# Kernel optimization log

Hardware: AMD Instinct MI355X
Metric: run time of the kernel (lower is better)

Reference implementation:

```python
import jax, jax.numpy as jnp
import numpy as np
from jax import lax

EPS = 1e-5  # GroupNorm eps (torch default)

def _silu(x):
    return x * jax.nn.sigmoid(x)

def _conv1x1(x, w, b):
    # x: (N, Ci, H, W), w: (Co, Ci), b: (Co,)
    return jnp.einsum('oi,nihw->nohw', w, x) + b[None, :, None, None]

def _conv3x3(x, w, b):
    # x: (N, Ci, H, W), w: (Co, Ci, 3, 3)
    y = lax.conv_general_dilated(x, w, window_strides=(1, 1), padding='SAME',
                                 dimension_numbers=('NCHW', 'OIHW', 'NCHW'))
    return y + b[None, :, None, None]

def setup_inputs() -> dict:
    key = jax.random.key(0)
    ks = jax.random.split(key, 6)
    B, C, H, W = 32, 512, 64, 64
    cg = 16
    return {
        'x': jax.random.normal(ks[0], (B, C, H, W), dtype=jnp.float32),
        'w1': jax.random.normal(ks[1], (cg, cg), dtype=jnp.float32) * 0.1,
        'b1': jnp.zeros((cg,), jnp.float32),
        'wh': jax.random.normal(ks[2], (cg, cg), dtype=jnp.float32) * 0.1,
        'bh': jnp.zeros((cg,), jnp.float32),
        'ww': jax.random.normal(ks[3], (cg, cg), dtype=jnp.float32) * 0.1,
        'bw': jnp.zeros((cg,), jnp.float32),
        'w3': jax.random.normal(ks[4], (cg, cg, 3, 3), dtype=jnp.float32) * 0.1,
        'b3': jnp.zeros((cg,), jnp.float32),
        'gamma': jnp.ones((cg,), jnp.float32),
        'beta': jnp.zeros((cg,), jnp.float32),
    }

def reference(x, w1, b1, wh, bh, ww, bw, w3, b3, gamma, beta):
    b, c, h, w = x.shape
    cg = w1.shape[0]
    g = c // cg
    n = b * g
    hw = h * w
    xg = x.reshape(n, cg, h, w)
    # directional pooling: (N, cg, H, 1) and (N, cg, W, 1)
    x_h = jnp.mean(xg, axis=3, keepdims=True)
    x_w = jnp.transpose(jnp.mean(xg, axis=2, keepdims=True), (0, 1, 3, 2))
    y = jnp.concatenate([x_h, x_w], axis=2)            # (N, cg, H+W, 1)
    y = _silu(_conv1x1(y, w1, b1))
    y_h, y_w = y[:, :, :h, :], y[:, :, h:, :]
    y_w = jnp.transpose(y_w, (0, 1, 3, 2))             # (N, cg, 1, W)
    a_h = jax.nn.sigmoid(_conv1x1(y_h, wh, bh))        # (N, cg, H, 1)
    a_w = jax.nn.sigmoid(_conv1x1(y_w, ww, bw))        # (N, cg, 1, W)
    x1 = xg * a_h * a_w
    # GroupNorm(num_groups=1): normalize over (cg, H, W) per sample
    mu = jnp.mean(x1, axis=(1, 2, 3), keepdims=True)
    var = jnp.var(x1, axis=(1, 2, 3), keepdims=True)
    x1 = (x1 - mu) * lax.rsqrt(var + EPS)
    x1 = x1 * gamma[None, :, None, None] + beta[None, :, None, None]
    x3 = _silu(_conv3x3(xg, w3, b3))
    A1 = jax.nn.softmax(x1.reshape(n, cg, hw), axis=-1)
    A3 = jax.nn.softmax(x3.reshape(n, cg, hw), axis=-1)
    v1 = jnp.mean(x1, axis=(2, 3))                     # (N, cg)
    v3 = jnp.mean(x3, axis=(2, 3))                     # (N, cg)
    s1 = jnp.einsum('nc,ncp->np', v1, A3)              # (N, HW)
    s2 = jnp.einsum('nc,ncp->np', v3, A1)
    s = jax.nn.sigmoid(s1 + s2).reshape(n, 1, h, w)
    out = (xg * s).reshape(b, c, h, w)
    return out
```

## Files before the change

### kernel.cpp

```cpp
#include <hip/hip_runtime.h>


typedef short bf16x8 __attribute__((ext_vector_type(8)));
typedef float f32x4 __attribute__((ext_vector_type(4)));

__device__ __forceinline__ unsigned short f2bf(float f) {
    union { float f; unsigned int u; } v; v.f = f;
    unsigned int u = v.u;
    u += 0x7fffu + ((u >> 16) & 1u);
    return (unsigned short)(u >> 16);
}
__device__ __forceinline__ float bf2f(unsigned short h) {
    union { unsigned int u; float f; } v; v.u = ((unsigned int)h) << 16;
    return v.f;
}
__device__ __forceinline__ float sigm(float v) { return 1.0f / (1.0f + __expf(-v)); }

#define XIDX(h1,w1,c) ((((h1)*2 + ((c)>>3))*66 + (w1))*8 + ((c)&7))

__global__ __launch_bounds__(512) void ema_fused(
    const float* __restrict__ x,
    const float* __restrict__ w1, const float* __restrict__ b1,
    const float* __restrict__ wh, const float* __restrict__ bh,
    const float* __restrict__ ww, const float* __restrict__ bw,
    const float* __restrict__ w3, const float* __restrict__ b3,
    const float* __restrict__ gamma, const float* __restrict__ beta,
    float* __restrict__ out)
{
    const int n   = blockIdx.x;
    const int tid = threadIdx.x;
    const int lane = tid & 63;
    const int wv   = tid >> 6;
    const int qd   = lane >> 4;
    const int col  = lane & 15;

    const float* xg = x + (size_t)n * 65536;
    unsigned int* ob = (unsigned int*)out + (size_t)n * 65536;

    __shared__ unsigned short sX[69696];
    __shared__ float sG[2048];
    __shared__ float sRedA[128], sRedB[128], sRedC[128], sRedD[128];
    __shared__ float sS1[16], sSQ[16], sMn[16], sMx[16], sM3[16], sS3[16];
    __shared__ float sA[16], sB1[16], sQ1[16], sQ3[16];
    __shared__ float sScal[2];

    for (int i = tid; i < 34848; i += 512) ((unsigned int*)sX)[i] = 0u;
    __syncthreads();
    for (int e = tid; e < 32768; e += 512) {
        int c2 = e & 7, w = (e >> 3) & 63, r = e >> 9;
        float v0 = xg[(2*c2)*4096 + r*64 + w];
        float v1 = xg[(2*c2+1)*4096 + r*64 + w];
        unsigned int pk = (unsigned int)f2bf(v0) | ((unsigned int)f2bf(v1) << 16);
        ((unsigned int*)sX)[XIDX(r+1, w+1, 2*c2) >> 1] = pk;
    }
    __syncthreads();

    if (tid < 256) {
        int half = tid & 1;
        int idx  = tid >> 1;
        int isCol = idx >> 6;
        int rc = idx & 63;
        float acc[8] = {0,0,0,0,0,0,0,0};
        for (int t = 0; t < 64; ++t) {
            int hh = isCol ? (t + 1) : (rc + 1);
            int wwi = isCol ? (rc + 1) : (t + 1);
            const bf16x8 v = *(const bf16x8*)&sX[XIDX(hh, wwi, half*8)];
            #pragma unroll
            for (int j = 0; j < 8; ++j) acc[j] += bf2f((unsigned short)v[j]);
        }
        #pragma unroll
        for (int j = 0; j < 8; ++j)
            sG[isCol*1024 + (half*8+j)*64 + rc] = acc[j] * (1.0f/64.0f);
    }
    __syncthreads();

    {
        float yv[4];
        #pragma unroll
        for (int j = 0; j < 4; ++j) {
            int tsk = tid + j*512;
            int o = tsk & 15, q = tsk >> 4;
            float acc = b1[o];
            #pragma unroll
            for (int i = 0; i < 16; ++i)
                acc += w1[o*16 + i] * sG[((q>>6)<<10) + i*64 + (q & 63)];
            yv[j] = acc * sigm(acc);
        }
        __syncthreads();
        #pragma unroll
        for (int j = 0; j < 4; ++j) {
            int tsk = tid + j*512;
            int o = tsk & 15, q = tsk >> 4;
            sG[o*128 + q] = yv[j];
        }
    }
    __syncthreads();
    {
        float av[4];
        #pragma unroll
        for (int j = 0; j < 4; ++j) {
            int tsk = tid + j*512;
            int kind = tsk >> 10;
            int o = tsk & 15, pos = (tsk >> 4) & 63;
            const float* wm = kind ? ww : wh;
            float acc = kind ? bw[o] : bh[o];
            #pragma unroll
            for (int i = 0; i < 16; ++i)
                acc += wm[o*16 + i] * sG[i*128 + kind*64 + pos];
            av[j] = sigm(acc);
        }
        __syncthreads();
        #pragma unroll
        for (int j = 0; j < 4; ++j) {
            int tsk = tid + j*512;
            int kind = tsk >> 10, o = tsk & 15, pos = (tsk >> 4) & 63;
            sG[kind*1024 + o*64 + pos] = av[j];
        }
    }
    __syncthreads();

    {
        bf16x8 afr[5];
        int offs[5];
        #pragma unroll
        for (int mm = 0; mm < 5; ++mm) {
            int t = 2*mm + (qd >> 1);
            #pragma unroll
            for (int j = 0; j < 8; ++j) {
                int i = ((qd & 1) << 3) + j;
                float v = (t <= 8) ? w3[(col*16 + i)*9 + t] : 0.0f;
                afr[mm][j] = (short)f2bf(v);
            }
            int tb = (t > 8) ? 8 : t;
            int dy = tb/3 - 1, dx = tb - (tb/3)*3 - 1;
            offs[mm] = dy*1056 + dx*8;
        }
        float b3v[4];
        #pragma unroll
        for (int r = 0; r < 4; ++r) b3v[r] = b3[qd*4 + r];

        float tmax[4] = {-1e30f,-1e30f,-1e30f,-1e30f};
        float tsum[4] = {0.f,0.f,0.f,0.f};

        for (int k = 0; k < 32; ++k) {
            int tile = wv*32 + k;
            int h = tile >> 2, wq = tile & 3;
            int base = XIDX(h+1, wq*16 + col + 1, (qd & 1)*8);
            f32x4 acc = {0.f, 0.f, 0.f, 0.f};
            #pragma unroll
            for (int mm = 0; mm < 5; ++mm) {
                const bf16x8 bfr = *(const bf16x8*)&sX[base + offs[mm]];
                acc = __builtin_amdgcn_mfma_f32_16x16x32_bf16(afr[mm], bfr, acc, 0, 0, 0);
            }
            int p = h*64 + wq*16 + col;
            float xv[4];
            #pragma unroll
            for (int r = 0; r < 4; ++r) {
                float v = acc[r] + b3v[r];
                float sv = v * sigm(v);
                xv[r] = sv;
                tmax[r] = fmaxf(tmax[r], sv);
                tsum[r] += sv;
            }
            unsigned int u0 = (unsigned int)f2bf(xv[0]) | ((unsigned int)f2bf(xv[1]) << 16);
            unsigned int u1 = (unsigned int)f2bf(xv[2]) | ((unsigned int)f2bf(xv[3]) << 16);
            ob[(4*qd)*4096 + p]     = u0;
            ob[(4*qd + 2)*4096 + p] = u1;
        }
        #pragma unroll
        for (int m = 1; m < 16; m <<= 1) {
            #pragma unroll
            for (int r = 0; r < 4; ++r) {
                tmax[r] = fmaxf(tmax[r], __shfl_xor(tmax[r], m, 64));
                tsum[r] += __shfl_xor(tsum[r], m, 64);
            }
        }
        if (col == 0) {
            #pragma unroll
            for (int r = 0; r < 4; ++r) {
                sRedA[wv*16 + qd*4 + r] = tmax[r];
                sRedB[wv*16 + qd*4 + r] = tsum[r];
            }
        }
    }
    __syncthreads();
    if (tid < 16) {
        float mx = -1e30f, sm = 0.f;
        for (int v2 = 0; v2 < 8; ++v2) { mx = fmaxf(mx, sRedA[v2*16 + tid]); sm += sRedB[v2*16 + tid]; }
        sM3[tid] = mx; sS3[tid] = sm;
    }
    __syncthreads();

    {
        int half = tid & 1;
        int wq4  = (tid >> 1) & 3;
        int r    = tid >> 3;
        float ah8[8];
        #pragma unroll
        for (int j = 0; j < 8; ++j) ah8[j] = sG[(half*8+j)*64 + r];
        float s1[8], q1[8], mn[8], mx[8];
        #pragma unroll
        for (int j = 0; j < 8; ++j) { s1[j]=0.f; q1[j]=0.f; mn[j]=1e30f; mx[j]=-1e30f; }
        for (int wi = 0; wi < 16; ++wi) {
            int w = wq4*16 + wi;
            const bf16x8 v = *(const bf16x8*)&sX[XIDX(r+1, w+1, half*8)];
            #pragma unroll
            for (int j = 0; j < 8; ++j) {
                float aw = sG[1024 + (half*8+j)*64 + w];
                float x1 = bf2f((unsigned short)v[j]) * ah8[j] * aw;
                s1[j] += x1; q1[j] += x1*x1;
                mn[j] = fminf(mn[j], x1); mx[j] = fmaxf(mx[j], x1);
            }
        }
        #pragma unroll
        for (int m = 2; m < 64; m <<= 1) {
            #pragma unroll
            for (int j = 0; j < 8; ++j) {
                s1[j] += __shfl_xor(s1[j], m, 64);
                q1[j] += __shfl_xor(q1[j], m, 64);
                mn[j] = fminf(mn[j], __shfl_xor(mn[j], m, 64));
                mx[j] = fmaxf(mx[j], __shfl_xor(mx[j], m, 64));
            }
        }
        if ((lane >> 1) == 0) {
            #pragma unroll
            for (int j = 0; j < 8; ++j) {
                int c = half*8 + j;
                sRedA[wv*16 + c] = s1[j];
                sRedB[wv*16 + c] = q1[j];
                sRedC[wv*16 + c] = mn[j];
                sRedD[wv*16 + c] = mx[j];
            }
        }
    }
    __syncthreads();
    if (tid < 16) {
        float s=0.f, q=0.f, mn=1e30f, mx=-1e30f;
        for (int v2 = 0; v2 < 8; ++v2) {
            s += sRedA[v2*16+tid]; q += sRedB[v2*16+tid];
            mn = fminf(mn, sRedC[v2*16+tid]); mx = fmaxf(mx, sRedD[v2*16+tid]);
        }
        sS1[tid]=s; sSQ[tid]=q; sMn[tid]=mn; sMx[tid]=mx;
    }
    __syncthreads();
    if (tid == 0) {
        float S=0.f, Q=0.f;
        for (int c = 0; c < 16; ++c) { S += sS1[c]; Q += sSQ[c]; }
        float mu = S * (1.0f/65536.0f);
        float var = Q * (1.0f/65536.0f) - mu*mu;
        sScal[0] = mu; sScal[1] = rsqrtf(var + 1e-5f);
    }
    __syncthreads();
    if (tid < 16) {
        float mu = sScal[0], rstd = sScal[1];
        float a  = gamma[tid] * rstd;
        float bb = beta[tid] - mu * a;
        float m1 = (a >= 0.f) ? (a*sMx[tid] + bb) : (a*sMn[tid] + bb);
        sA[tid]  = a;
        sB1[tid] = bb - m1;
        sMn[tid] = a * (sS1[tid] * (1.0f/4096.0f)) + bb;
        sMx[tid] = sS3[tid] * (1.0f/4096.0f);
    }
    __syncthreads();

    {
        float z1[16], z3[16];
        #pragma unroll
        for (int c = 0; c < 16; ++c) { z1[c]=0.f; z3[c]=0.f; }
        for (int pp = 0; pp < 8; ++pp) {
            int p = pp*512 + tid;
            int h = p >> 6, w = p & 63;
            const bf16x8 v0 = *(const bf16x8*)&sX[XIDX(h+1, w+1, 0)];
            const bf16x8 v1 = *(const bf16x8*)&sX[XIDX(h+1, w+1, 8)];
            unsigned int xq[8];
            #pragma unroll
            for (int c2 = 0; c2 < 8; ++c2) xq[c2] = ob[(2*c2)*4096 + p];
            #pragma unroll
            for (int c = 0; c < 16; ++c) {
                float xv = bf2f((unsigned short)((c < 8) ? v0[c] : v1[c-8]));
                float g = sG[c*64 + h] * sG[1024 + c*64 + w];
                z1[c] += __expf(xv*g*sA[c] + sB1[c]);
                unsigned short ub = (unsigned short)((c & 1) ? (xq[c>>1] >> 16) : (xq[c>>1] & 0xffffu));
                z3[c] += __expf(bf2f(ub) - sM3[c]);
            }
        }
        #pragma unroll
        for (int m = 1; m < 64; m <<= 1) {
            #pragma unroll
            for (int c = 0; c < 16; ++c) {
                z1[c] += __shfl_xor(z1[c], m, 64);
                z3[c] += __shfl_xor(z3[c], m, 64);
            }
        }
        if (lane == 0) {
            #pragma unroll
            for (int c = 0; c < 16; ++c) { sRedA[wv*16 + c] = z1[c]; sRedB[wv*16 + c] = z3[c]; }
        }
    }
    __syncthreads();
    if (tid < 16) {
        float a1=0.f, a3=0.f;
        for (int v2 = 0; v2 < 8; ++v2) { a1 += sRedA[v2*16+tid]; a3 += sRedB[v2*16+tid]; }
        sQ1[tid] = sMx[tid] / a1;
        sQ3[tid] = sMn[tid] / a3;
    }
    __syncthreads();

    for (int pp = 0; pp < 8; ++pp) {
        int p = pp*512 + tid;
        int h = p >> 6, w = p & 63;
        const bf16x8 v0 = *(const bf16x8*)&sX[XIDX(h+1, w+1, 0)];
        const bf16x8 v1 = *(const bf16x8*)&sX[XIDX(h+1, w+1, 8)];
        unsigned int xq[8];
        #pragma unroll
        for (int c2 = 0; c2 < 8; ++c2) xq[c2] = ob[(2*c2)*4096 + p];
        float xf[16];
        #pragma unroll
        for (int c = 0; c < 16; ++c) xf[c] = xg[c*4096 + p];
        float z = 0.f;
        #pragma unroll
        for (int c = 0; c < 16; ++c) {
            float xv = bf2f((unsigned short)((c < 8) ? v0[c] : v1[c-8]));
            float g = sG[c*64 + h] * sG[1024 + c*64 + w];
            float e1 = __expf(xv*g*sA[c] + sB1[c]);
            unsigned short ub = (unsigned short)((c & 1) ? (xq[c>>1] >> 16) : (xq[c>>1] & 0xffffu));
            float e3 = __expf(bf2f(ub) - sM3[c]);
            z += sQ3[c]*e3 + sQ1[c]*e1;
        }
        float s = 1.0f / (1.0f + __expf(-z));
        #pragma unroll
        for (int c = 0; c < 16; ++c)
            ob[c*4096 + p] = __float_as_uint(xf[c] * s);
    }
}

extern "C" void kernel_launch(void* const* d_in, const int* in_sizes, int n_in,
                              void* d_out, int out_size, void* d_ws, size_t ws_size,
                              hipStream_t stream) {
    const float* x     = (const float*)d_in[0];
    const float* w1    = (const float*)d_in[1];
    const float* b1    = (const float*)d_in[2];
    const float* wh    = (const float*)d_in[3];
    const float* bh    = (const float*)d_in[4];
    const float* ww    = (const float*)d_in[5];
    const float* bw    = (const float*)d_in[6];
    const float* w3    = (const float*)d_in[7];
    const float* b3    = (const float*)d_in[8];
    const float* gamma = (const float*)d_in[9];
    const float* beta  = (const float*)d_in[10];
    hipLaunchKernelGGL(ema_fused, dim3(1024), dim3(512), 0, stream,
                       x, w1, b1, wh, bh, ww, bw, w3, b3, gamma, beta, (float*)d_out);
}
```

Baseline: 725.3 us.

## Recompute 3x3 conv via MFMA instead of spilling bf16 x3 to global; 1024-thread blocks

The conv3x3+SiLU result is no longer written to the output buffer as bf16 and re-read twice. Instead the MFMA convolution is recomputed from LDS in the softmax-denominator pass and the final pass. Block size doubles to 1024 threads, with the pooling and reductions split across more threads. A transposed padded sAW table avoids bank conflicts. This trades extra MFMA work for removing global round-trips, at the cost of register pressure under the larger block.

Result: slower. 751.4 us (+3.6%).

```diff
diff --git a/kernel.cpp b/kernel.cpp
--- a/kernel.cpp
+++ b/kernel.cpp
@@ -2,6 +2,7 @@
 
 
 typedef short bf16x8 __attribute__((ext_vector_type(8)));
+typedef short bf16x4 __attribute__((ext_vector_type(4)));
 typedef float f32x4 __attribute__((ext_vector_type(4)));
 
 __device__ __forceinline__ unsigned short f2bf(float f) {
@@ -18,7 +19,7 @@
 
 #define XIDX(h1,w1,c) ((((h1)*2 + ((c)>>3))*66 + (w1))*8 + ((c)&7))
 
-__global__ __launch_bounds__(512) void ema_fused(
+__global__ __launch_bounds__(1024, 4) void ema_fused(
     const float* __restrict__ x,
     const float* __restrict__ w1, const float* __restrict__ b1,
     const float* __restrict__ wh, const float* __restrict__ bh,
@@ -33,20 +34,24 @@
     const int wv   = tid >> 6;
     const int qd   = lane >> 4;
     const int col  = lane & 15;
+    const int cBase = qd * 4;
 
     const float* xg = x + (size_t)n * 65536;
     unsigned int* ob = (unsigned int*)out + (size_t)n * 65536;
 
     __shared__ unsigned short sX[69696];
     __shared__ float sG[2048];
-    __shared__ float sRedA[128], sRedB[128], sRedC[128], sRedD[128];
+    __shared__ float sAW[1088];
+    __shared__ float sRedA[256], sRedB[256], sRedC[256], sRedD[256];
     __shared__ float sS1[16], sSQ[16], sMn[16], sMx[16], sM3[16], sS3[16];
     __shared__ float sA[16], sB1[16], sQ1[16], sQ3[16];
     __shared__ float sScal[2];
 
-    for (int i = tid; i < 34848; i += 512) ((unsigned int*)sX)[i] = 0u;
-    __syncthreads();
-    for (int e = tid; e < 32768; e += 512) {
+    for (int i = tid; i < 34848; i += 1024) ((unsigned int*)sX)[i] = 0u;
+    __syncthreads();
+    #pragma unroll
+    for (int it = 0; it < 32; ++it) {
+        int e = tid + it * 1024;
         int c2 = e & 7, w = (e >> 3) & 63, r = e >> 9;
         float v0 = xg[(2*c2)*4096 + r*64 + w];
         float v1 = xg[(2*c2+1)*4096 + r*64 + w];
@@ -55,30 +60,37 @@
     }
     __syncthreads();
 
-    if (tid < 256) {
-        int half = tid & 1;
-        int idx  = tid >> 1;
+    {
+        int task = tid >> 2, sub = tid & 3;
+        int half = task & 1;
+        int idx  = task >> 1;
         int isCol = idx >> 6;
         int rc = idx & 63;
         float acc[8] = {0,0,0,0,0,0,0,0};
-        for (int t = 0; t < 64; ++t) {
-            int hh = isCol ? (t + 1) : (rc + 1);
+        for (int tt = 0; tt < 16; ++tt) {
+            int t = sub*16 + tt;
+            int hh  = isCol ? (t + 1) : (rc + 1);
             int wwi = isCol ? (rc + 1) : (t + 1);
             const bf16x8 v = *(const bf16x8*)&sX[XIDX(hh, wwi, half*8)];
             #pragma unroll
             for (int j = 0; j < 8; ++j) acc[j] += bf2f((unsigned short)v[j]);
         }
         #pragma unroll
-        for (int j = 0; j < 8; ++j)
-            sG[isCol*1024 + (half*8+j)*64 + rc] = acc[j] * (1.0f/64.0f);
-    }
-    __syncthreads();
-
-    {
-        float yv[4];
-        #pragma unroll
-        for (int j = 0; j < 4; ++j) {
-            int tsk = tid + j*512;
+        for (int m = 1; m < 4; m <<= 1)
+            #pragma unroll
+            for (int j = 0; j < 8; ++j) acc[j] += __shfl_xor(acc[j], m, 64);
+        if (sub == 0)
+            #pragma unroll
+            for (int j = 0; j < 8; ++j)
+                sG[isCol*1024 + (half*8+j)*64 + rc] = acc[j] * (1.0f/64.0f);
+    }
+    __syncthreads();
+
+    {
+        float yv[2];
+        #pragma unroll
+        for (int j = 0; j < 2; ++j) {
+            int tsk = tid + j*1024;
             int o = tsk & 15, q = tsk >> 4;
             float acc = b1[o];
             #pragma unroll
@@ -88,18 +100,18 @@
         }
         __syncthreads();
         #pragma unroll
-        for (int j = 0; j < 4; ++j) {
-            int tsk = tid + j*512;
+        for (int j = 0; j < 2; ++j) {
+            int tsk = tid + j*1024;
             int o = tsk & 15, q = tsk >> 4;
             sG[o*128 + q] = yv[j];
         }
     }
     __syncthreads();
     {
-        float av[4];
-        #pragma unroll
-        for (int j = 0; j < 4; ++j) {
-            int tsk = tid + j*512;
+        float av[2];
+        #pragma unroll
+        for (int j = 0; j < 2; ++j) {
+            int tsk = tid + j*1024;
             int kind = tsk >> 10;
             int o = tsk & 15, pos = (tsk >> 4) & 63;
             const float* wm = kind ? ww : wh;
@@ -111,39 +123,39 @@
         }
         __syncthreads();
         #pragma unroll
-        for (int j = 0; j < 4; ++j) {
-            int tsk = tid + j*512;
+        for (int j = 0; j < 2; ++j) {
+            int tsk = tid + j*1024;
             int kind = tsk >> 10, o = tsk & 15, pos = (tsk >> 4) & 63;
-            sG[kind*1024 + o*64 + pos] = av[j];
-        }
-    }
-    __syncthreads();
-
-    {
-        bf16x8 afr[5];
-        int offs[5];
-        #pragma unroll
-        for (int mm = 0; mm < 5; ++mm) {
-            int t = 2*mm + (qd >> 1);
-            #pragma unroll
-            for (int j = 0; j < 8; ++j) {
-                int i = ((qd & 1) << 3) + j;
-                float v = (t <= 8) ? w3[(col*16 + i)*9 + t] : 0.0f;
-                afr[mm][j] = (short)f2bf(v);
-            }
-            int tb = (t > 8) ? 8 : t;
-            int dy = tb/3 - 1, dx = tb - (tb/3)*3 - 1;
-            offs[mm] = dy*1056 + dx*8;
-        }
-        float b3v[4];
-        #pragma unroll
-        for (int r = 0; r < 4; ++r) b3v[r] = b3[qd*4 + r];
-
+            if (kind == 0) sG[o*64 + pos] = av[j];
+            else           sAW[pos*17 + o] = av[j];
+        }
+    }
+    __syncthreads();
+
+    bf16x8 afr[5];
+    int offs[5];
+    #pragma unroll
+    for (int mm = 0; mm < 5; ++mm) {
+        int t = 2*mm + (qd >> 1);
+        #pragma unroll
+        for (int j = 0; j < 8; ++j) {
+            int i = ((qd & 1) << 3) + j;
+            float v = (t <= 8) ? w3[(col*16 + i)*9 + t] : 0.0f;
+            afr[mm][j] = (short)f2bf(v);
+        }
+        int tb = (t > 8) ? 8 : t;
+        int dy = tb/3 - 1, dx = tb - (tb/3)*3 - 1;
+        offs[mm] = dy*1056 + dx*8;
+    }
+    float b3v[4];
+    #pragma unroll
+    for (int r = 0; r < 4; ++r) b3v[r] = b3[cBase + r];
+
+    {
         float tmax[4] = {-1e30f,-1e30f,-1e30f,-1e30f};
         float tsum[4] = {0.f,0.f,0.f,0.f};
-
-        for (int k = 0; k < 32; ++k) {
-            int tile = wv*32 + k;
+        for (int k = 0; k < 16; ++k) {
+            int tile = wv*16 + k;
             int h = tile >> 2, wq = tile & 3;
             int base = XIDX(h+1, wq*16 + col + 1, (qd & 1)*8);
             f32x4 acc = {0.f, 0.f, 0.f, 0.f};
@@ -152,68 +164,59 @@
                 const bf16x8 bfr = *(const bf16x8*)&sX[base + offs[mm]];
                 acc = __builtin_amdgcn_mfma_f32_16x16x32_bf16(afr[mm], bfr, acc, 0, 0, 0);
             }
-            int p = h*64 + wq*16 + col;
-            float xv[4];
             #pragma unroll
             for (int r = 0; r < 4; ++r) {
                 float v = acc[r] + b3v[r];
                 float sv = v * sigm(v);
-                xv[r] = sv;
                 tmax[r] = fmaxf(tmax[r], sv);
                 tsum[r] += sv;
             }
-            unsigned int u0 = (unsigned int)f2bf(xv[0]) | ((unsigned int)f2bf(xv[1]) << 16);
-            unsigned int u1 = (unsigned int)f2bf(xv[2]) | ((unsigned int)f2bf(xv[3]) << 16);
-            ob[(4*qd)*4096 + p]     = u0;
-            ob[(4*qd + 2)*4096 + p] = u1;
-        }
-        #pragma unroll
-        for (int m = 1; m < 16; m <<= 1) {
+        }
+        #pragma unroll
+        for (int m = 1; m < 16; m <<= 1)
             #pragma unroll
             for (int r = 0; r < 4; ++r) {
                 tmax[r] = fmaxf(tmax[r], __shfl_xor(tmax[r], m, 64));
                 tsum[r] += __shfl_xor(tsum[r], m, 64);
             }
-        }
-        if (col == 0) {
-            #pragma unroll
-            for (int r = 0; r < 4; ++r) {
-                sRedA[wv*16 + qd*4 + r] = tmax[r];
-                sRedB[wv*16 + qd*4 + r] = tsum[r];
-            }
-        }
+        if (col == 0)
+            #pragma unroll
+            for (int r = 0; r < 4; ++r) {
+                sRedA[wv*16 + cBase + r] = tmax[r];
+                sRedB[wv*16 + cBase + r] = tsum[r];
+            }
     }
     __syncthreads();
     if (tid < 16) {
         float mx = -1e30f, sm = 0.f;
-        for (int v2 = 0; v2 < 8; ++v2) { mx = fmaxf(mx, sRedA[v2*16 + tid]); sm += sRedB[v2*16 + tid]; }
+        for (int v2 = 0; v2 < 16; ++v2) { mx = fmaxf(mx, sRedA[v2*16 + tid]); sm += sRedB[v2*16 + tid]; }
         sM3[tid] = mx; sS3[tid] = sm;
     }
     __syncthreads();
 
     {
         int half = tid & 1;
-        int wq4  = (tid >> 1) & 3;
-        int r    = tid >> 3;
+        int wq8  = (tid >> 1) & 7;
+        int r    = tid >> 4;
         float ah8[8];
         #pragma unroll
         for (int j = 0; j < 8; ++j) ah8[j] = sG[(half*8+j)*64 + r];
         float s1[8], q1[8], mn[8], mx[8];
         #pragma unroll
         for (int j = 0; j < 8; ++j) { s1[j]=0.f; q1[j]=0.f; mn[j]=1e30f; mx[j]=-1e30f; }
-        for (int wi = 0; wi < 16; ++wi) {
-            int w = wq4*16 + wi;
+        for (int wi = 0; wi < 8; ++wi) {
+            int w = wq8*8 + wi;
             const bf16x8 v = *(const bf16x8*)&sX[XIDX(r+1, w+1, half*8)];
             #pragma unroll
             for (int j = 0; j < 8; ++j) {
-                float aw = sG[1024 + (half*8+j)*64 + w];
+                float aw = sAW[w*17 + half*8 + j];
                 float x1 = bf2f((unsigned short)v[j]) * ah8[j] * aw;
                 s1[j] += x1; q1[j] += x1*x1;
                 mn[j] = fminf(mn[j], x1); mx[j] = fmaxf(mx[j], x1);
             }
         }
         #pragma unroll
-        for (int m = 2; m < 64; m <<= 1) {
+        for (int m = 2; m < 64; m <<= 1)
             #pragma unroll
             for (int j = 0; j < 8; ++j) {
                 s1[j] += __shfl_xor(s1[j], m, 64);
@@ -221,8 +224,7 @@
                 mn[j] = fminf(mn[j], __shfl_xor(mn[j], m, 64));
                 mx[j] = fmaxf(mx[j], __shfl_xor(mx[j], m, 64));
             }
-        }
-        if ((lane >> 1) == 0) {
+        if ((lane & 62) == 0) {
             #pragma unroll
             for (int j = 0; j < 8; ++j) {
                 int c = half*8 + j;
@@ -236,7 +238,7 @@
     __syncthreads();
     if (tid < 16) {
         float s=0.f, q=0.f, mn=1e30f, mx=-1e30f;
-        for (int v2 = 0; v2 < 8; ++v2) {
+        for (int v2 = 0; v2 < 16; ++v2) {
             s += sRedA[v2*16+tid]; q += sRedB[v2*16+tid];
             mn = fminf(mn, sRedC[v2*16+tid]); mx = fmaxf(mx, sRedD[v2*16+tid]);
         }
@@ -263,74 +265,95 @@
     }
     __syncthreads();
 
-    {
-        float z1[16], z3[16];
-        #pragma unroll
-        for (int c = 0; c < 16; ++c) { z1[c]=0.f; z3[c]=0.f; }
-        for (int pp = 0; pp < 8; ++pp) {
-            int p = pp*512 + tid;
-            int h = p >> 6, w = p & 63;
-            const bf16x8 v0 = *(const bf16x8*)&sX[XIDX(h+1, w+1, 0)];
-            const bf16x8 v1 = *(const bf16x8*)&sX[XIDX(h+1, w+1, 8)];
-            unsigned int xq[8];
-            #pragma unroll
-            for (int c2 = 0; c2 < 8; ++c2) xq[c2] = ob[(2*c2)*4096 + p];
-            #pragma unroll
-            for (int c = 0; c < 16; ++c) {
-                float xv = bf2f((unsigned short)((c < 8) ? v0[c] : v1[c-8]));
-                float g = sG[c*64 + h] * sG[1024 + c*64 + w];
-                z1[c] += __expf(xv*g*sA[c] + sB1[c]);
-                unsigned short ub = (unsigned short)((c & 1) ? (xq[c>>1] >> 16) : (xq[c>>1] & 0xffffu));
-                z3[c] += __expf(bf2f(ub) - sM3[c]);
-            }
-        }
-        #pragma unroll
-        for (int m = 1; m < 64; m <<= 1) {
-            #pragma unroll
-            for (int c = 0; c < 16; ++c) {
-                z1[c] += __shfl_xor(z1[c], m, 64);
-                z3[c] += __shfl_xor(z3[c], m, 64);
-            }
-        }
-        if (lane == 0) {
-            #pragma unroll
-            for (int c = 0; c < 16; ++c) { sRedA[wv*16 + c] = z1[c]; sRedB[wv*16 + c] = z3[c]; }
-        }
+    float aC[4], bC[4], m3C[4];
+    #pragma unroll
+    for (int r = 0; r < 4; ++r) { aC[r]=sA[cBase+r]; bC[r]=sB1[cBase+r]; m3C[r]=sM3[cBase+r]; }
+
+    {
+        float z1l[4] = {0,0,0,0}, z3l[4] = {0,0,0,0};
+        for (int k = 0; k < 16; ++k) {
+            int tile = wv*16 + k;
+            int h = tile >> 2, wq = tile & 3;
+            int w = wq*16 + col;
+            int base = XIDX(h+1, w+1, (qd & 1)*8);
+            f32x4 acc = {0.f, 0.f, 0.f, 0.f};
+            #pragma unroll
+            for (int mm = 0; mm < 5; ++mm) {
+                const bf16x8 bfr = *(const bf16x8*)&sX[base + offs[mm]];
+                acc = __builtin_amdgcn_mfma_f32_16x16x32_bf16(afr[mm], bfr, acc, 0, 0, 0);
+            }
+            const bf16x4 xv4 = *(const bf16x4*)&sX[XIDX(h+1, w+1, cBase)];
+            #pragma unroll
+            for (int r = 0; r < 4; ++r) {
+                float v = acc[r] + b3v[r];
+                float x3 = v * sigm(v);
+                z3l[r] += __expf(x3 - m3C[r]);
+                float g = sG[(cBase+r)*64 + h] * sAW[w*17 + cBase + r];
+                float xv = bf2f((unsigned short)xv4[r]);
+                z1l[r] += __expf(xv*g*aC[r] + bC[r]);
+            }
+        }
+        #pragma unroll
+        for (int m = 1; m < 16; m <<= 1)
+            #pragma unroll
+            for (int r = 0; r < 4; ++r) {
+                z1l[r] += __shfl_xor(z1l[r], m, 64);
+                z3l[r] += __shfl_xor(z3l[r], m, 64);
+            }
+        if (col == 0)
+            #pragma unroll
+            for (int r = 0; r < 4; ++r) {
+                sRedA[wv*16 + cBase + r] = z1l[r];
+                sRedB[wv*16 + cBase + r] = z3l[r];
+            }
     }
     __syncthreads();
     if (tid < 16) {
         float a1=0.f, a3=0.f;
-        for (int v2 = 0; v2 < 8; ++v2) { a1 += sRedA[v2*16+tid]; a3 += sRedB[v2*16+tid]; }
+        for (int v2 = 0; v2 < 16; ++v2) { a1 += sRedA[v2*16+tid]; a3 += sRedB[v2*16+tid]; }
         sQ1[tid] = sMx[tid] / a1;
         sQ3[tid] = sMn[tid] / a3;
     }
     __syncthreads();
 
-    for (int pp = 0; pp < 8; ++pp) {
-        int p = pp*512 + tid;
-        int h = p >> 6, w = p & 63;
-        const bf16x8 v0 = *(const bf16x8*)&sX[XIDX(h+1, w+1, 0)];
-        const bf16x8 v1 = *(const bf16x8*)&sX[XIDX(h+1, w+1, 8)];
-        unsigned int xq[8];
-        #pragma unroll
-        for (int c2 = 0; c2 < 8; ++c2) xq[c2] = ob[(2*c2)*4096 + p];
-        float xf[16];
-        #pragma unroll
-        for (int c = 0; c < 16; ++c) xf[c] = xg[c*4096 + p];
-        float z = 0.f;
-        #pragma unroll
-        for (int c = 0; c < 16; ++c) {
-            float xv = bf2f((unsigned short)((c < 8) ? v0[c] : v1[c-8]));
-            float g = sG[c*64 + h] * sG[1024 + c*64 + w];
-            float e1 = __expf(xv*g*sA[c] + sB1[c]);
-            unsigned short ub = (unsigned short)((c & 1) ? (xq[c>>1] >> 16) : (xq[c>>1] & 0xffffu));
-            float e3 = __expf(bf2f(ub) - sM3[c]);
-            z += sQ3[c]*e3 + sQ1[c]*e1;
-        }
-        float s = 1.0f / (1.0f + __expf(-z));
-        #pragma unroll
-        for (int c = 0; c < 16; ++c)
-            ob[c*4096 + p] = __float_as_uint(xf[c] * s);
+    {
+        float q1C[4], q3C[4];
+        #pragma unroll
+        for (int r = 0; r < 4; ++r) { q1C[r]=sQ1[cBase+r]; q3C[r]=sQ3[cBase+r]; }
+        for (int k = 0; k < 16; ++k) {
+            int tile = wv*16 + k;
+            int h = tile >> 2, wq = tile & 3;
+            int w = wq*16 + col;
+            int p = h*64 + w;
+            float xf[4];
+            #pragma unroll
+            for (int r = 0; r < 4; ++r) xf[r] = xg[(cBase+r)*4096 + p];
+            int base = XIDX(h+1, w+1, (qd & 1)*8);
+            f32x4 acc = {0.f, 0.f, 0.f, 0.f};
+            #pragma unroll
+            for (int mm = 0; mm < 5; ++mm) {
+                const bf16x8 bfr = *(const bf16x8*)&sX[base + offs[mm]];
+                acc = __builtin_amdgcn_mfma_f32_16x16x32_bf16(afr[mm], bfr, acc, 0, 0, 0);
+            }
+            const bf16x4 xv4 = *(const bf16x4*)&sX[XIDX(h+1, w+1, cBase)];
+            float part = 0.f;
+            #pragma unroll
+            for (int r = 0; r < 4; ++r) {
+                float v = acc[r] + b3v[r];
+                float x3 = v * sigm(v);
+                float e3 = __expf(x3 - m3C[r]);
+                float g = sG[(cBase+r)*64 + h] * sAW[w*17 + cBase + r];
+                float xv = bf2f((unsigned short)xv4[r]);
+                float e1 = __expf(xv*g*aC[r] + bC[r]);
+                part += q3C[r]*e3 + q1C[r]*e1;
+            }
+            part += __shfl_xor(part, 16, 64);
+            part += __shfl_xor(part, 32, 64);
+            float s = 1.0f / (1.0f + __expf(-part));
+            #pragma unroll
+            for (int r = 0; r < 4; ++r)
+                ob[(cBase+r)*4096 + p] = __float_as_uint(xf[r] * s);
+        }
     }
 }
 
@@ -348,6 +371,6 @@
     const float* b3    = (const float*)d_in[8];
     const float* gamma = (const float*)d_in[9];
     const float* beta  = (const float*)d_in[10];
-    hipLaunchKernelGGL(ema_fused, dim3(1024), dim3(512), 0, stream,
+    hipLaunchKernelGGL(ema_fused, dim3(1024), dim3(1024), 0, stream,
                        x, w1, b1, wh, bh, ww, bw, w3, b3, gamma, beta, (float*)d_out);
 }
```
